# Kernel optimization log

Measured on AMD Instinct MI355X. Metric: run time of the kernel, lower is better.

The kernel has to match this reference:

```python
import jax, jax.numpy as jnp
import numpy as np

NX, NY, NZ = 432, 496, 1
VX, VY, VZ = 0.16, 0.16, 4.0
XOFF = VX / 2 + 0.0
YOFF = VY / 2 + (-39.68)
ZOFF = VZ / 2 + (-3.0)
GRID = NZ * NX * NY
P, NPT, B = 100000, 32, 8
EPS = 1e-3


def setup_inputs() -> dict:
    key = jax.random.key(0)
    k1, k2, k3, k4 = jax.random.split(key, 4)
    voxels = jax.random.normal(k1, (P, NPT, 4), dtype=jnp.float32)
    num_points = jax.random.randint(k2, (P,), 1, NPT + 1, dtype=jnp.int32)
    b = jax.random.randint(k3, (P,), 0, B, dtype=jnp.int32)
    # unique BEV cells (17 coprime with GRID, P < GRID) -> deterministic scatter
    cell = (jnp.arange(P, dtype=jnp.int32) * 17) % GRID
    y = cell // NX
    x = cell % NX
    coords = jnp.stack([b, jnp.zeros_like(b), y, x], axis=1)  # [P,4] (b,z,y,x)
    W = jax.random.normal(k4, (64, 10), dtype=jnp.float32) * 0.1
    gamma = jnp.ones((64,), dtype=jnp.float32)
    beta = jnp.zeros((64,), dtype=jnp.float32)
    return {"voxels": voxels, "num_points": num_points, "coords": coords,
            "W": W, "gamma": gamma, "beta": beta}


def reference(voxels, num_points, coords, W, gamma, beta):
    cf = coords.astype(voxels.dtype)
    npf = num_points.astype(voxels.dtype)
    # cluster feature: offset from pillar mean
    points_mean = voxels[:, :, :3].sum(axis=1, keepdims=True) / npf[:, None, None]
    f_cluster = voxels[:, :, :3] - points_mean
    # center feature: offset from voxel center
    cx = cf[:, 3, None] * VX + XOFF
    cy = cf[:, 2, None] * VY + YOFF
    cz = cf[:, 1, None] * VZ + ZOFF
    f_center = jnp.stack([voxels[:, :, 0] - cx,
                          voxels[:, :, 1] - cy,
                          voxels[:, :, 2] - cz], axis=-1)
    feat = jnp.concatenate([voxels, f_cluster, f_center], axis=-1)  # [P,N,10]
    mask = (jnp.arange(NPT, dtype=jnp.int32)[None, :] < num_points[:, None])
    feat = feat * mask.astype(feat.dtype)[:, :, None]
    # linear(10->64, no bias) + BatchNorm1d (batch stats, biased var) + relu
    x = jnp.einsum('pnf,cf->pnc', feat, W)  # [P,N,64]
    mean = x.mean(axis=(0, 1))
    var = ((x - mean) ** 2).mean(axis=(0, 1))
    x = (x - mean) * jax.lax.rsqrt(var + EPS) * gamma + beta
    x = jax.nn.relu(x)
    pillars = x.max(axis=1)  # [P,64]
    idx = coords[:, 1] + coords[:, 2] * NX + coords[:, 3]
    bev = jnp.zeros((B, GRID, 64), dtype=pillars.dtype)
    bev = bev.at[coords[:, 0], idx].set(pillars)
    bev = jnp.transpose(bev, (0, 2, 1))  # [B,64,GRID]
    return bev.reshape(B, 64 * NZ, NY, NX)
```

## Files before the change

kernel.cpp:

```cpp
#include <hip/hip_runtime.h>

typedef unsigned short u16;

#define NXg 432
#define NYg 496
#define GRIDg (NXg*NYg)
#define NPTg 32
#define Bg 8
#define CHg 64
#define NSLOT 32

__device__ __forceinline__ float bf2f(u16 u){
    union { unsigned int i; float f; } x; x.i = ((unsigned int)u) << 16; return x.f;
}
__device__ __forceinline__ u16 f2bf(float f){
    union { float f; unsigned int i; } x; x.f = f;
    unsigned int i = x.i + 0x7FFFu + ((x.i >> 16) & 1u);
    return (u16)(i >> 16);
}
__device__ __forceinline__ bool is_bf16(const void* gamma){
    return ((*(const unsigned*)gamma) & 0xFFFFu) != 0u;
}
__device__ __forceinline__ float rdlane(float v, int k){
    return __int_as_float(__builtin_amdgcn_readlane(__float_as_int(v), k));
}

__global__ __launch_bounds__(256) void pfe_init(int* __restrict__ map, float* __restrict__ chsum){
    int t = blockIdx.x*256 + threadIdx.x;
    ((int4*)map)[t] = make_int4(-1,-1,-1,-1);
    if (t < (NSLOT*128)/4) ((float4*)chsum)[t] = make_float4(0.f,0.f,0.f,0.f);
}

__global__ __launch_bounds__(256) void pfe_pillar(
    const void* __restrict__ vox, const int* __restrict__ nump,
    const int* __restrict__ coords, const void* __restrict__ Wv,
    const void* __restrict__ gv,
    u16* __restrict__ pmax, u16* __restrict__ pmin,
    int* __restrict__ map, float* __restrict__ chsum,
    int P, int nwaves)
{
    const bool isbf = is_bf16(gv);
    int lane = threadIdx.x & 63;
    int wid  = (blockIdx.x*256 + threadIdx.x) >> 6;
    int n    = lane & 31;

    float w4,w5,w6,w7,w8,w9, wp0,wp1,wp2,wp3;
    {
        float w[10];
#pragma unroll
        for (int j=0;j<10;j++)
            w[j] = isbf ? bf2f(((const u16*)Wv)[lane*10 + j]) : ((const float*)Wv)[lane*10 + j];
        wp0 = w[0]+w[4]+w[7];
        wp1 = w[1]+w[5]+w[8];
        wp2 = w[2]+w[6]+w[9];
        wp3 = w[3];
        w4=w[4]; w5=w[5]; w6=w[6]; w7=w[7]; w8=w[8]; w9=w[9];
    }

    float sx = 0.f, sx2 = 0.f;

    for (int p = wid; p < P; p += nwaves) {
        int np = nump[p];
        int4 cc = *(const int4*)(coords + 4*p);
        float4 pt;
        if (isbf){
            ushort4 raw = *(const ushort4*)((const u16*)vox + ((size_t)p*NPTg + n)*4);
            pt = make_float4(bf2f(raw.x), bf2f(raw.y), bf2f(raw.z), bf2f(raw.w));
        } else {
            pt = *(const float4*)((const float*)vox + ((size_t)p*NPTg + n)*4);
        }

        float s0 = pt.x, s1 = pt.y, s2 = pt.z;
#pragma unroll
        for (int m = 1; m < 64; m <<= 1){
            s0 += __shfl_xor(s0, m, 64);
            s1 += __shfl_xor(s1, m, 64);
            s2 += __shfl_xor(s2, m, 64);
        }
        float inv = 0.5f / (float)np;
        float m0 = s0*inv, m1 = s1*inv, m2 = s2*inv;
        float ccx = (float)cc.w * 0.16f + 0.08f;
        float ccy = (float)cc.z * 0.16f + (0.08f - 39.68f);
        float ccz = (float)cc.y * 4.0f  + (2.0f - 3.0f);
        float d = -(m0*w4 + m1*w5 + m2*w6 + ccx*w7 + ccy*w8 + ccz*w9);

        float qmx = -3e38f, qmn = 3e38f, sq = 0.f, sq2 = 0.f;
        for (int k = 0; k < np; k++){
            float ax = rdlane(pt.x, k);
            float ay = rdlane(pt.y, k);
            float az = rdlane(pt.z, k);
            float aw = rdlane(pt.w, k);
            float q = fmaf(ax, wp0, fmaf(ay, wp1, fmaf(az, wp2, aw*wp3)));
            qmx = fmaxf(qmx, q);
            qmn = fminf(qmn, q);
            sq += q;
            sq2 = fmaf(q, q, sq2);
        }

        float npf = (float)np;
        sx  += sq + npf*d;
        sx2 += sq2 + d*(2.f*sq + npf*d);

        float fmx = qmx + d, fmn = qmn + d;
        if (np < NPTg){ fmx = fmaxf(fmx, 0.f); fmn = fminf(fmn, 0.f); }
        pmax[(size_t)p*CHg + lane] = f2bf(fmx);
        pmin[(size_t)p*CHg + lane] = f2bf(fmn);
        if (lane == 0) map[cc.x*GRIDg + cc.z*NXg + cc.w] = p;
    }

    float* slot = chsum + (blockIdx.x & (NSLOT-1))*128;
    atomicAdd(slot + lane, sx);
    atomicAdd(slot + 64 + lane, sx2);
}

__global__ __launch_bounds__(64) void pfe_stats(
    const float* __restrict__ chsum,
    const void* __restrict__ gv, const void* __restrict__ bv,
    float* __restrict__ sb, int P)
{
    const bool isbf = is_bf16(gv);
    int t = threadIdx.x;
    float S = 0.f, S2 = 0.f;
    for (int sl = 0; sl < NSLOT; sl++){
        S  += chsum[sl*128 + t];
        S2 += chsum[sl*128 + 64 + t];
    }
    float cnt = (float)P * (float)NPTg;
    float mean = S / cnt;
    float var  = S2 / cnt - mean*mean;
    float g  = isbf ? bf2f(((const u16*)gv)[t]) : ((const float*)gv)[t];
    float be = isbf ? bf2f(((const u16*)bv)[t]) : ((const float*)bv)[t];
    float sc = g * rsqrtf(var + 1e-3f);
    float bi = be - mean*sc;
    sb[t] = sc; sb[64 + t] = bi;
    ((int*)sb)[128 + t] = (sc >= 0.f) ? 0 : P*CHg*2;
}

__global__ __launch_bounds__(192) void pfe_gather(
    const int* __restrict__ map, const u16* __restrict__ pmax,
    const float* __restrict__ sb, const void* __restrict__ gv,
    void* __restrict__ out)
{
    const bool isbf = is_bf16(gv);
    int b  = blockIdx.y;
    int px = blockIdx.x*384 + threadIdx.x*2;
    int2 m2 = *(const int2*)(map + (size_t)b*GRIDg + px);
    bool v0 = m2.x >= 0, v1 = m2.y >= 0;
    int o0 = v0 ? m2.x*(CHg*2) : 0;
    int o1 = v1 ? m2.y*(CHg*2) : 0;
    const char* pb = (const char*)pmax;

#pragma unroll
    for (int c = 0; c < CHg; c++){
        float sc = sb[c], bi = sb[64 + c];
        int off = __builtin_amdgcn_readfirstlane(((const int*)sb)[128 + c]);
        const char* base = pb + off;
        float x0 = bf2f(*(const u16*)(base + o0 + c*2));
        float x1 = bf2f(*(const u16*)(base + o1 + c*2));
        float r0 = v0 ? fmaxf(fmaf(sc, x0, bi), 0.f) : 0.f;
        float r1 = v1 ? fmaxf(fmaf(sc, x1, bi), 0.f) : 0.f;
        size_t obase = ((size_t)(b*CHg + c))*GRIDg + px;
        if (isbf){
            unsigned pk = (unsigned)f2bf(r0) | ((unsigned)f2bf(r1) << 16);
            *(unsigned*)((u16*)out + obase) = pk;
        } else {
            *(float2*)((float*)out + obase) = make_float2(r0, r1);
        }
    }
}

extern "C" void kernel_launch(void* const* d_in, const int* in_sizes, int n_in,
                              void* d_out, int out_size, void* d_ws, size_t ws_size,
                              hipStream_t stream)
{
    const void* vox   = d_in[0];
    const int* nump   = (const int*)d_in[1];
    const int* coords = (const int*)d_in[2];
    const void* Wv    = d_in[3];
    const void* gv    = d_in[4];
    const void* bv    = d_in[5];
    int P = in_sizes[1];

    float* chsum = (float*)d_ws;
    float* sb    = (float*)((char*)d_ws + 16384);
    u16*   pmax  = (u16*)((char*)d_ws + 32768);
    u16*   pmin  = pmax + (size_t)P*CHg;
    int*   map   = (int*)(pmin + (size_t)P*CHg);

    int initThreads = (Bg*GRIDg)/4;
    pfe_init<<<initThreads/256, 256, 0, stream>>>(map, chsum);

    int blocks1 = 2048;
    pfe_pillar<<<blocks1, 256, 0, stream>>>(vox, nump, coords, Wv, gv, pmax, pmin, map, chsum, P, blocks1*4);

    pfe_stats<<<1, 64, 0, stream>>>(chsum, gv, bv, sb, P);

    dim3 g3(GRIDg/384, Bg);
    pfe_gather<<<g3, 192, 0, stream>>>(map, pmax, sb, gv, d_out);
}
```

Baseline: 555.7 us.

## Store single gamma-selected extreme per pillar and vectorize gather reads

The pillar kernel now picks max or min per channel from the sign of gamma, which it reads directly, and writes one bf16 array instead of separate max and min arrays. This halves the intermediate writes and removes the per-channel offset lookup in the gather. The gather now loads 32 channels per pillar with 16-byte vector loads and splits channels across a new grid dimension, and the point loop is unrolled by four. The selection assumes rsqrt(var+eps) is positive, so the sign of the BN scale equals the sign of gamma.

```diff
diff --git a/kernel.cpp b/kernel.cpp
--- a/kernel.cpp
+++ b/kernel.cpp
@@ -35,8 +35,7 @@
     const void* __restrict__ vox, const int* __restrict__ nump,
     const int* __restrict__ coords, const void* __restrict__ Wv,
     const void* __restrict__ gv,
-    u16* __restrict__ pmax, u16* __restrict__ pmin,
-    int* __restrict__ map, float* __restrict__ chsum,
+    u16* __restrict__ pv, int* __restrict__ map, float* __restrict__ chsum,
     int P, int nwaves)
 {
     const bool isbf = is_bf16(gv);
@@ -45,6 +44,7 @@
     int n    = lane & 31;
 
     float w4,w5,w6,w7,w8,w9, wp0,wp1,wp2,wp3;
+    bool gsel;
     {
         float w[10];
 #pragma unroll
@@ -55,6 +55,8 @@
         wp2 = w[2]+w[6]+w[9];
         wp3 = w[3];
         w4=w[4]; w5=w[5]; w6=w[6]; w7=w[7]; w8=w[8]; w9=w[9];
+        float g = isbf ? bf2f(((const u16*)gv)[lane]) : ((const float*)gv)[lane];
+        gsel = (g >= 0.f);
     }
 
     float sx = 0.f, sx2 = 0.f;
@@ -85,7 +87,22 @@
         float d = -(m0*w4 + m1*w5 + m2*w6 + ccx*w7 + ccy*w8 + ccz*w9);
 
         float qmx = -3e38f, qmn = 3e38f, sq = 0.f, sq2 = 0.f;
-        for (int k = 0; k < np; k++){
+        int k = 0;
+        for (; k + 4 <= np; k += 4){
+#pragma unroll
+            for (int u = 0; u < 4; u++){
+                float ax = rdlane(pt.x, k+u);
+                float ay = rdlane(pt.y, k+u);
+                float az = rdlane(pt.z, k+u);
+                float aw = rdlane(pt.w, k+u);
+                float q = fmaf(ax, wp0, fmaf(ay, wp1, fmaf(az, wp2, aw*wp3)));
+                qmx = fmaxf(qmx, q);
+                qmn = fminf(qmn, q);
+                sq += q;
+                sq2 = fmaf(q, q, sq2);
+            }
+        }
+        for (; k < np; k++){
             float ax = rdlane(pt.x, k);
             float ay = rdlane(pt.y, k);
             float az = rdlane(pt.z, k);
@@ -103,8 +120,7 @@
 
         float fmx = qmx + d, fmn = qmn + d;
         if (np < NPTg){ fmx = fmaxf(fmx, 0.f); fmn = fminf(fmn, 0.f); }
-        pmax[(size_t)p*CHg + lane] = f2bf(fmx);
-        pmin[(size_t)p*CHg + lane] = f2bf(fmn);
+        pv[(size_t)p*CHg + lane] = f2bf(gsel ? fmx : fmn);
         if (lane == 0) map[cc.x*GRIDg + cc.z*NXg + cc.w] = p;
     }
 
@@ -131,40 +147,50 @@
     float g  = isbf ? bf2f(((const u16*)gv)[t]) : ((const float*)gv)[t];
     float be = isbf ? bf2f(((const u16*)bv)[t]) : ((const float*)bv)[t];
     float sc = g * rsqrtf(var + 1e-3f);
-    float bi = be - mean*sc;
-    sb[t] = sc; sb[64 + t] = bi;
-    ((int*)sb)[128 + t] = (sc >= 0.f) ? 0 : P*CHg*2;
+    sb[t] = sc; sb[64 + t] = be - mean*sc;
 }
 
 __global__ __launch_bounds__(192) void pfe_gather(
-    const int* __restrict__ map, const u16* __restrict__ pmax,
+    const int* __restrict__ map, const u16* __restrict__ pv,
     const float* __restrict__ sb, const void* __restrict__ gv,
     void* __restrict__ out)
 {
     const bool isbf = is_bf16(gv);
-    int b  = blockIdx.y;
+    int b  = blockIdx.z;
+    int c0 = blockIdx.y * 32;
     int px = blockIdx.x*384 + threadIdx.x*2;
     int2 m2 = *(const int2*)(map + (size_t)b*GRIDg + px);
     bool v0 = m2.x >= 0, v1 = m2.y >= 0;
-    int o0 = v0 ? m2.x*(CHg*2) : 0;
-    int o1 = v1 ? m2.y*(CHg*2) : 0;
-    const char* pb = (const char*)pmax;
-
-#pragma unroll
-    for (int c = 0; c < CHg; c++){
-        float sc = sb[c], bi = sb[64 + c];
-        int off = __builtin_amdgcn_readfirstlane(((const int*)sb)[128 + c]);
-        const char* base = pb + off;
-        float x0 = bf2f(*(const u16*)(base + o0 + c*2));
-        float x1 = bf2f(*(const u16*)(base + o1 + c*2));
-        float r0 = v0 ? fmaxf(fmaf(sc, x0, bi), 0.f) : 0.f;
-        float r1 = v1 ? fmaxf(fmaf(sc, x1, bi), 0.f) : 0.f;
-        size_t obase = ((size_t)(b*CHg + c))*GRIDg + px;
+    int p0 = v0 ? m2.x : 0;
+    int p1 = v1 ? m2.y : 0;
+
+    uint4 R0[4], R1[4];
+    const uint4* r0p = (const uint4*)(pv + (size_t)p0*CHg + c0);
+    const uint4* r1p = (const uint4*)(pv + (size_t)p1*CHg + c0);
+#pragma unroll
+    for (int i = 0; i < 4; i++){ R0[i] = r0p[i]; R1[i] = r1p[i]; }
+
+    unsigned mask01 = (v0 ? 0x0000FFFFu : 0u) | (v1 ? 0xFFFF0000u : 0u);
+
+#pragma unroll
+    for (int j = 0; j < 32; j++){
+        float sc = sb[c0 + j];
+        float bi = sb[64 + c0 + j];
+        unsigned d0 = ((const unsigned*)R0)[j >> 1];
+        unsigned d1 = ((const unsigned*)R1)[j >> 1];
+        float x0 = __uint_as_float((j & 1) ? (d0 & 0xFFFF0000u) : (d0 << 16));
+        float x1 = __uint_as_float((j & 1) ? (d1 & 0xFFFF0000u) : (d1 << 16));
+        float r0 = fmaxf(fmaf(sc, x0, bi), 0.f);
+        float r1 = fmaxf(fmaf(sc, x1, bi), 0.f);
+        size_t obase = ((size_t)(b*CHg + c0 + j))*GRIDg + px;
         if (isbf){
-            unsigned pk = (unsigned)f2bf(r0) | ((unsigned)f2bf(r1) << 16);
+            unsigned pk = ((unsigned)f2bf(r0) | ((unsigned)f2bf(r1) << 16)) & mask01;
             *(unsigned*)((u16*)out + obase) = pk;
         } else {
-            *(float2*)((float*)out + obase) = make_float2(r0, r1);
+            float2 o;
+            o.x = v0 ? r0 : 0.f;
+            o.y = v1 ? r1 : 0.f;
+            *(float2*)((float*)out + obase) = o;
         }
     }
 }
@@ -183,18 +209,17 @@
 
     float* chsum = (float*)d_ws;
     float* sb    = (float*)((char*)d_ws + 16384);
-    u16*   pmax  = (u16*)((char*)d_ws + 32768);
-    u16*   pmin  = pmax + (size_t)P*CHg;
-    int*   map   = (int*)(pmin + (size_t)P*CHg);
+    u16*   pv    = (u16*)((char*)d_ws + 32768);
+    int*   map   = (int*)((char*)pv + (size_t)P*CHg*2);
 
     int initThreads = (Bg*GRIDg)/4;
     pfe_init<<<initThreads/256, 256, 0, stream>>>(map, chsum);
 
     int blocks1 = 2048;
-    pfe_pillar<<<blocks1, 256, 0, stream>>>(vox, nump, coords, Wv, gv, pmax, pmin, map, chsum, P, blocks1*4);
+    pfe_pillar<<<blocks1, 256, 0, stream>>>(vox, nump, coords, Wv, gv, pv, map, chsum, P, blocks1*4);
 
     pfe_stats<<<1, 64, 0, stream>>>(chsum, gv, bv, sb, P);
 
-    dim3 g3(GRIDg/384, Bg);
-    pfe_gather<<<g3, 192, 0, stream>>>(map, pmax, sb, gv, d_out);
-}
+    dim3 g3(GRIDg/384, 2, Bg);
+    pfe_gather<<<g3, 192, 0, stream>>>(map, pv, sb, gv, d_out);
+}
```

Result: faster. 538.4 us (-3.1%).
